# Performance work log

Measured on AMD Instinct MI355X. Metric: run time of the kernel, lower is better.

## Reference

```python
import jax, jax.numpy as jnp
import numpy as np

POP, D_IN, D_OUT, BATCH = 128, 1024, 1024, 256


def setup_inputs() -> dict:
    key = jax.random.key(0)
    kx, kw = jax.random.split(key)
    x = jax.random.normal(kx, (BATCH, POP, D_IN), dtype=jnp.float32)
    # matches torch init: randn * 0.02, bias zeros
    weight = jax.random.normal(kw, (POP, D_OUT, D_IN), dtype=jnp.float32) * 0.02
    bias = jnp.zeros((POP, D_OUT), dtype=jnp.float32)
    return {"x": x, "weight": weight, "bias": bias}


def reference(x, weight, bias):
    # Per-population linear: out[b,p,o] = sum_i x[b,p,i] * weight[p,o,i] + bias[p,o]
    # Broadcast weights across batch in-kernel instead of materializing
    # the [batch, pop, out, in] expansion the torch code creates.
    out = jnp.einsum("bpi,poi->bpo", x, weight)
    return out + bias[None, :, :]
```

## Files before the change

### kernel.cpp

```cpp
#include <hip/hip_runtime.h>

#define POP   128
#define BATCH 256
#define DIN   1024
#define DOUT  1024

#define BM 128
#define BN 128
#define BK 32
#define LDS_K (BK + 8)

typedef __attribute__((ext_vector_type(8))) short  short8v;
typedef __attribute__((ext_vector_type(4))) short  short4v;
typedef __attribute__((ext_vector_type(4))) float  float4v;

static __device__ __forceinline__ short f2bf(float f) {
    unsigned u = __builtin_bit_cast(unsigned, f);
    u += 0x7fffu + ((u >> 16) & 1u);
    return (short)(u >> 16);
}

__global__ __launch_bounds__(256, 2)
void pop_linear_kernel(const float* __restrict__ x,
                       const float* __restrict__ w,
                       const float* __restrict__ bias,
                       float* __restrict__ out) {
    __shared__ short As[BM * LDS_K];
    __shared__ short Bs[BN * LDS_K];

    const int bid = blockIdx.x;
    const int p      = bid >> 4;
    const int m_tile = (bid >> 3) & 1;
    const int n_tile = bid & 7;

    const int tid    = threadIdx.x;
    const int lane   = tid & 63;
    const int wave   = tid >> 6;
    const int wm     = wave >> 1;
    const int wn     = wave & 1;
    const int lane15 = lane & 15;
    const int quad   = lane >> 4;

    const int m_base = m_tile * BM;
    const int n_base = n_tile * BN;

    const int srow = tid >> 3;
    const int scol = (tid & 7) * 4;

    const float* Ag = x + (size_t)(m_base + srow) * (POP * DIN) + (size_t)p * DIN + scol;
    const float* Bg = w + (size_t)p * ((size_t)DOUT * DIN) + (size_t)(n_base + srow) * DIN + scol;

    float4v acc[4][4];
    #pragma unroll
    for (int i = 0; i < 4; ++i)
        #pragma unroll
        for (int j = 0; j < 4; ++j)
            acc[i][j] = (float4v){0.f, 0.f, 0.f, 0.f};

    for (int kt = 0; kt < DIN / BK; ++kt) {
        const int k0 = kt * BK;

        float4v av[4], bv[4];
        #pragma unroll
        for (int pass = 0; pass < 4; ++pass) {
            av[pass] = *(const float4v*)(Ag + (size_t)(pass * 32) * (POP * DIN) + k0);
            bv[pass] = *(const float4v*)(Bg + (size_t)(pass * 32) * DIN + k0);
        }

        __syncthreads();

        #pragma unroll
        for (int pass = 0; pass < 4; ++pass) {
            short4v a4, b4;
            #pragma unroll
            for (int e = 0; e < 4; ++e) {
                a4[e] = f2bf(av[pass][e]);
                b4[e] = f2bf(bv[pass][e]);
            }
            *(short4v*)&As[(pass * 32 + srow) * LDS_K + scol] = a4;
            *(short4v*)&Bs[(pass * 32 + srow) * LDS_K + scol] = b4;
        }

        __syncthreads();

        short8v af[4], bf[4];
        #pragma unroll
        for (int i = 0; i < 4; ++i) {
            af[i] = *(const short8v*)&As[(wm * 64 + i * 16 + lane15) * LDS_K + quad * 8];
            bf[i] = *(const short8v*)&Bs[(wn * 64 + i * 16 + lane15) * LDS_K + quad * 8];
        }

        #pragma unroll
        for (int i = 0; i < 4; ++i)
            #pragma unroll
            for (int j = 0; j < 4; ++j)
                acc[i][j] = __builtin_amdgcn_mfma_f32_16x16x32_bf16(af[i], bf[j], acc[i][j], 0, 0, 0);
    }

    const float* bp = bias + (size_t)p * DOUT;
    float bj[4];
    #pragma unroll
    for (int j = 0; j < 4; ++j)
        bj[j] = bp[n_base + wn * 64 + j * 16 + lane15];

    #pragma unroll
    for (int i = 0; i < 4; ++i) {
        #pragma unroll
        for (int r = 0; r < 4; ++r) {
            const int m = m_base + wm * 64 + i * 16 + quad * 4 + r;
            float* orow = out + (size_t)m * (POP * DOUT) + (size_t)p * DOUT;
            #pragma unroll
            for (int j = 0; j < 4; ++j) {
                const int n = n_base + wn * 64 + j * 16 + lane15;
                orow[n] = acc[i][j][r] + bj[j];
            }
        }
    }
}

extern "C" void kernel_launch(void* const* d_in, const int* in_sizes, int n_in,
                              void* d_out, int out_size, void* d_ws, size_t ws_size,
                              hipStream_t stream) {
    const float* x    = (const float*)d_in[0];
    const float* w    = (const float*)d_in[1];
    const float* bias = (const float*)d_in[2];
    float* out        = (float*)d_out;

    const int grid = POP * (BATCH / BM) * (DOUT / BN);
    pop_linear_kernel<<<grid, 256, 0, stream>>>(x, w, bias, out);
}
```

Baseline: 986.9 us.

## Enlarge K tile, prefetch next tile into registers, swizzle LDS layout

```diff
diff --git a/kernel.cpp b/kernel.cpp
--- a/kernel.cpp
+++ b/kernel.cpp
@@ -7,8 +7,8 @@
 
 #define BM 128
 #define BN 128
-#define BK 32
-#define LDS_K (BK + 8)
+#define BK 128
+#define NKT (DIN / BK)
 
 typedef __attribute__((ext_vector_type(8))) short  short8v;
 typedef __attribute__((ext_vector_type(4))) short  short4v;
@@ -20,13 +20,17 @@
     return (short)(u >> 16);
 }
 
+static __device__ __forceinline__ void lds_barrier() {
+    asm volatile("s_waitcnt lgkmcnt(0)\n\ts_barrier" ::: "memory");
+}
+
 __global__ __launch_bounds__(256, 2)
 void pop_linear_kernel(const float* __restrict__ x,
                        const float* __restrict__ w,
                        const float* __restrict__ bias,
                        float* __restrict__ out) {
-    __shared__ short As[BM * LDS_K];
-    __shared__ short Bs[BN * LDS_K];
+    __shared__ short As[BM * BK];
+    __shared__ short Bs[BN * BK];
 
     const int bid = blockIdx.x;
     const int p      = bid >> 4;
@@ -44,11 +48,13 @@
     const int m_base = m_tile * BM;
     const int n_base = n_tile * BN;
 
-    const int srow = tid >> 3;
-    const int scol = (tid & 7) * 4;
+    const int srow8 = tid >> 5;
+    const int scolf = (tid & 31) * 4;
 
-    const float* Ag = x + (size_t)(m_base + srow) * (POP * DIN) + (size_t)p * DIN + scol;
-    const float* Bg = w + (size_t)p * ((size_t)DOUT * DIN) + (size_t)(n_base + srow) * DIN + scol;
+    const float* Ag = x + (size_t)(m_base + srow8) * (POP * DIN) + (size_t)p * DIN + scolf;
+    const float* Bg = w + (size_t)p * ((size_t)DOUT * DIN) + (size_t)(n_base + srow8) * DIN + scolf;
+
+    const int swz = (scolf * 2) ^ (srow8 << 4);
 
     float4v acc[4][4];
     #pragma unroll
@@ -57,44 +63,60 @@
         for (int j = 0; j < 4; ++j)
             acc[i][j] = (float4v){0.f, 0.f, 0.f, 0.f};
 
-    for (int kt = 0; kt < DIN / BK; ++kt) {
-        const int k0 = kt * BK;
+    float4v avr[16], bvr[16];
 
-        float4v av[4], bv[4];
-        #pragma unroll
-        for (int pass = 0; pass < 4; ++pass) {
-            av[pass] = *(const float4v*)(Ag + (size_t)(pass * 32) * (POP * DIN) + k0);
-            bv[pass] = *(const float4v*)(Bg + (size_t)(pass * 32) * DIN + k0);
-        }
+    const int frx = (lane15 & 7) << 4;
+    const char* Ac = (const char*)As;
+    const char* Bc = (const char*)Bs;
 
-        __syncthreads();
+    #pragma unroll
+    for (int ps = 0; ps < 16; ++ps) {
+        avr[ps] = *(const float4v*)(Ag + (size_t)(ps * 8) * (POP * DIN));
+        bvr[ps] = *(const float4v*)(Bg + (size_t)(ps * 8) * DIN);
+    }
+
+    #pragma unroll 1
+    for (int kt = 0; kt < NKT; ++kt) {
+        lds_barrier();
 
         #pragma unroll
-        for (int pass = 0; pass < 4; ++pass) {
+        for (int ps = 0; ps < 16; ++ps) {
             short4v a4, b4;
             #pragma unroll
             for (int e = 0; e < 4; ++e) {
-                a4[e] = f2bf(av[pass][e]);
-                b4[e] = f2bf(bv[pass][e]);
+                a4[e] = f2bf(avr[ps][e]);
+                b4[e] = f2bf(bvr[ps][e]);
             }
-            *(short4v*)&As[(pass * 32 + srow) * LDS_K + scol] = a4;
-            *(short4v*)&Bs[(pass * 32 + srow) * LDS_K + scol] = b4;
+            *(short4v*)((char*)As + (ps * 8 + srow8) * 256 + swz) = a4;
+            *(short4v*)((char*)Bs + (ps * 8 + srow8) * 256 + swz) = b4;
         }
 
-        __syncthreads();
+        lds_barrier();
 
-        short8v af[4], bf[4];
-        #pragma unroll
-        for (int i = 0; i < 4; ++i) {
-            af[i] = *(const short8v*)&As[(wm * 64 + i * 16 + lane15) * LDS_K + quad * 8];
-            bf[i] = *(const short8v*)&Bs[(wn * 64 + i * 16 + lane15) * LDS_K + quad * 8];
+        if (kt + 1 < NKT) {
+            const size_t k0 = (size_t)(kt + 1) * BK;
+            #pragma unroll
+            for (int ps = 0; ps < 16; ++ps) {
+                avr[ps] = *(const float4v*)(Ag + (size_t)(ps * 8) * (POP * DIN) + k0);
+                bvr[ps] = *(const float4v*)(Bg + (size_t)(ps * 8) * DIN + k0);
+            }
         }
 
         #pragma unroll
-        for (int i = 0; i < 4; ++i)
+        for (int kk = 0; kk < 4; ++kk) {
+            const int cb = (kk * 64 + quad * 16) ^ frx;
+            short8v bfr[4];
             #pragma unroll
             for (int j = 0; j < 4; ++j)
-                acc[i][j] = __builtin_amdgcn_mfma_f32_16x16x32_bf16(af[i], bf[j], acc[i][j], 0, 0, 0);
+                bfr[j] = *(const short8v*)(Bc + (wn * 64 + j * 16 + lane15) * 256 + cb);
+            #pragma unroll
+            for (int i = 0; i < 4; ++i) {
+                short8v afr = *(const short8v*)(Ac + (wm * 64 + i * 16 + lane15) * 256 + cb);
+                #pragma unroll
+                for (int j = 0; j < 4; ++j)
+                    acc[i][j] = __builtin_amdgcn_mfma_f32_16x16x32_bf16(afr, bfr[j], acc[i][j], 0, 0, 0);
+            }
+        }
     }
 
     const float* bp = bias + (size_t)p * DOUT;
```

Result: faster. 872.0 us (-11.6%).
